# Performance work log

Hardware: AMD Instinct MI355X
Metric: run time of the kernel (lower is better)

## Reference

```python
import jax, jax.numpy as jnp
import numpy as np

B, V, L, D, H, W = 4, 2, 8192, 768, 12, 512  # batch, views, seq, d_model, heads, window


def _layernorm(x, g, b, eps=1e-5):
    # matches torch LayerNorm computed in fp32 then cast back
    x32 = x.astype(jnp.float32)
    m = x32.mean(-1, keepdims=True)
    v = ((x32 - m) ** 2).mean(-1, keepdims=True)
    return ((x32 - m) * jax.lax.rsqrt(v + eps) * g + b).astype(x.dtype)


def _mha(q_in, k_in, v_in, wqkv, bqkv, wo, bo, h):
    # torch nn.MultiheadAttention (eval mode, no mask). inputs [..., S, d]
    d = q_in.shape[-1]
    hd = d // h
    scale = 1.0 / np.sqrt(hd)
    q = (q_in @ wqkv[:d].T + bqkv[:d]).reshape(*q_in.shape[:-1], h, hd)
    k = (k_in @ wqkv[d:2 * d].T + bqkv[d:2 * d]).reshape(*k_in.shape[:-1], h, hd)
    v = (v_in @ wqkv[2 * d:].T + bqkv[2 * d:]).reshape(*v_in.shape[:-1], h, hd)
    scores = jnp.einsum('...qhd,...khd->...hqk', q, k) * scale
    a = jax.nn.softmax(scores, axis=-1)
    o = jnp.einsum('...hqk,...khd->...qhd', a, v).reshape(q_in.shape)
    return o @ wo.T + bo


def reference(x, ln1_g, ln1_b, ln2_g, ln2_b,
              a1_wqkv, a1_bqkv, a1_wo, a1_bo,
              a2_wqkv, a2_bqkv, a2_wo, a2_bo,
              fc_w, fc_b, proj_w, proj_b, index):
    b, v, l, c = x.shape
    y = _layernorm(x, ln1_g, ln1_b)
    shifted = (index % 2 == 1)  # index is a static Python int
    xs = jnp.roll(x, W // 2, axis=2) if shifted else x
    p = l // W
    xw = xs.reshape(b, v, p, W, c)  # window partition (only x is rolled, as in source)
    yw = y.reshape(b, v, p, W, c)
    # cross-view windowed attention: Q=norm view i, K=norm view j, V=raw view i
    v1 = _mha(yw[:, 0], yw[:, 1], xw[:, 0], a1_wqkv, a1_bqkv, a1_wo, a1_bo, H)
    v2 = _mha(yw[:, 1], yw[:, 0], xw[:, 1], a2_wqkv, a2_bqkv, a2_wo, a2_bo, H)
    att = jnp.stack([v1, v2], axis=1).reshape(b, v, l, c)
    if shifted:
        att = jnp.roll(att, -(W // 2), axis=2)
    x = x + att
    y2 = _layernorm(x, ln2_g, ln2_b)
    h = y2 @ fc_w.T + fc_b
    h = h * jax.nn.sigmoid(1.702 * h)  # fast GELU
    return x + (h @ proj_w.T + proj_b)


def setup_inputs() -> dict:
    key = jax.random.key(0)
    ks = jax.random.split(key, 10)
    s = 0.02
    return {
        'x': jax.random.normal(ks[0], (B, V, L, D), jnp.float32),
        'ln1_g': jnp.ones((D,), jnp.float32),
        'ln1_b': jnp.zeros((D,), jnp.float32),
        'ln2_g': jnp.ones((D,), jnp.float32),
        'ln2_b': jnp.zeros((D,), jnp.float32),
        'a1_wqkv': jax.random.normal(ks[1], (3 * D, D), jnp.float32) * s,
        'a1_bqkv': jnp.zeros((3 * D,), jnp.float32),
        'a1_wo': jax.random.normal(ks[2], (D, D), jnp.float32) * s,
        'a1_bo': jnp.zeros((D,), jnp.float32),
        'a2_wqkv': jax.random.normal(ks[3], (3 * D, D), jnp.float32) * s,
        'a2_bqkv': jnp.zeros((3 * D,), jnp.float32),
        'a2_wo': jax.random.normal(ks[4], (D, D), jnp.float32) * s,
        'a2_bo': jnp.zeros((D,), jnp.float32),
        'fc_w': jax.random.normal(ks[5], (4 * D, D), jnp.float32) * s,
        'fc_b': jnp.zeros((4 * D,), jnp.float32),
        'proj_w': jax.random.normal(ks[6], (D, 4 * D), jnp.float32) * s,
        'proj_b': jnp.zeros((D,), jnp.float32),
        'index': 0,
    }
```

## Files before the change

### kernel.cpp

```cpp
#include <hip/hip_runtime.h>
#include <hip/hip_bf16.h>

typedef __bf16 bf16x8 __attribute__((ext_vector_type(8)));
typedef float  f32x4  __attribute__((ext_vector_type(4)));
typedef short  s16x4  __attribute__((ext_vector_type(4)));
typedef unsigned short u16;

#define L2E 1.44269504088896f

static __device__ __forceinline__ u16 f2bf(float f) {
  unsigned u = __builtin_bit_cast(unsigned, f);
  u += 0x7fffu + ((u >> 16) & 1u);
  return (u16)(u >> 16);
}

static __device__ __forceinline__ void gld_lds16(const void* g, void* l) {
  __builtin_amdgcn_global_load_lds((const __attribute__((address_space(1))) unsigned*)g,
                                   (__attribute__((address_space(3))) unsigned*)l, 16, 0, 0);
}

__global__ __launch_bounds__(256)
void cvtk(const float* __restrict__ s, u16* __restrict__ d, int n) {
  const int i = (blockIdx.x * 256 + threadIdx.x) * 4;
  if (i >= n) return;
  const float4 f = *(const float4*)(s + i);
  s16x4 p;
  p[0] = (short)f2bf(f.x); p[1] = (short)f2bf(f.y);
  p[2] = (short)f2bf(f.z); p[3] = (short)f2bf(f.w);
  *(s16x4*)(d + i) = p;
}

__global__ __launch_bounds__(256)
void lnk(const float* __restrict__ x, const float* __restrict__ gw,
         const float* __restrict__ bw, u16* __restrict__ y,
         u16* __restrict__ xv, int viewmajor) {
  const int lane = threadIdx.x & 63;
  const int tok = blockIdx.x * 4 + (threadIdx.x >> 6);
  const float* xr = x + (size_t)tok * 768;
  float4 v[3];
  float s = 0.f, sq = 0.f;
#pragma unroll
  for (int j = 0; j < 3; ++j) {
    v[j] = *(const float4*)(xr + j * 256 + lane * 4);
    s  += v[j].x + v[j].y + v[j].z + v[j].w;
    sq += v[j].x * v[j].x + v[j].y * v[j].y + v[j].z * v[j].z + v[j].w * v[j].w;
  }
#pragma unroll
  for (int o = 1; o < 64; o <<= 1) { s += __shfl_xor(s, o); sq += __shfl_xor(sq, o); }
  const float mean = s * (1.f / 768.f);
  const float var  = sq * (1.f / 768.f) - mean * mean;
  const float rstd = rsqrtf(var + 1e-5f);
  size_t yrow = (size_t)tok;
  if (viewmajor) {
    const int b_ = tok >> 14, vv = (tok >> 13) & 1, l_ = tok & 8191;
    yrow = ((size_t)((vv << 2) + b_) << 13) + l_;
  }
#pragma unroll
  for (int j = 0; j < 3; ++j) {
    const float4 g4 = *(const float4*)(gw + j * 256 + lane * 4);
    const float4 b4 = *(const float4*)(bw + j * 256 + lane * 4);
    s16x4 py;
    py[0] = (short)f2bf((v[j].x - mean) * rstd * g4.x + b4.x);
    py[1] = (short)f2bf((v[j].y - mean) * rstd * g4.y + b4.y);
    py[2] = (short)f2bf((v[j].z - mean) * rstd * g4.z + b4.z);
    py[3] = (short)f2bf((v[j].w - mean) * rstd * g4.w + b4.w);
    *(s16x4*)(y + yrow * 768 + j * 256 + lane * 4) = py;
    if (xv) {
      s16x4 px;
      px[0] = (short)f2bf(v[j].x); px[1] = (short)f2bf(v[j].y);
      px[2] = (short)f2bf(v[j].z); px[3] = (short)f2bf(v[j].w);
      *(s16x4*)(xv + yrow * 768 + j * 256 + lane * 4) = px;
    }
  }
}

template<int MODE>
__global__ __launch_bounds__(512, 2)
void gemm_bt(const u16* __restrict__ A, const u16* __restrict__ B,
             const float* __restrict__ bias, void* __restrict__ Cp,
             int N, int K,
             const float* __restrict__ xres, const int* __restrict__ idxp,
             int vview) {
  __shared__ char lds[131072];
  const int t = threadIdx.x;
  const int lane = t & 63;
  const int wid = t >> 6;
  const int wm = wid >> 2, wn = wid & 3;

  const int cpx = gridDim.x >> 3;
  const int bid = (blockIdx.x & 7) * cpx + (blockIdx.x >> 3);

  const int Ntiles = N >> 8;
  const int PPB = Ntiles << 3;
  const int panel = bid / PPB;
  const int rem = bid - panel * PPB;
  const int nt = rem >> 3;
  const int mt = (panel << 3) + (rem & 7);

  const int ra = t >> 3;
  const int sc = ((t & 7) ^ (ra & 7)) << 3;
  const u16* Asrc = A + (size_t)(mt * 256 + ra) * K + sc;
  const u16* Bsrc = B + (size_t)(nt * 256 + ra) * K + sc;
  char* LA = (char*)lds;
  char* LB = (char*)lds + 65536;
  const int wdst = wid << 10;

  auto stageA = [&](int d, int kt) {
#pragma unroll
    for (int h = 0; h < 2; ++h) {
      const u16* s = Asrc + (size_t)kt * 64 + (size_t)(h * 128) * K;
      char* dst = LA + (d * 2 + h) * 16384 + wdst;
      gld_lds16(s, dst);
      gld_lds16(s + (size_t)64 * K, dst + 8192);
    }
  };
  auto stageB = [&](int d, int kt) {
#pragma unroll
    for (int h = 0; h < 2; ++h) {
      const u16* s = Bsrc + (size_t)kt * 64 + (size_t)(h * 128) * K;
      char* dst = LB + (d * 2 + h) * 16384 + wdst;
      gld_lds16(s, dst);
      gld_lds16(s + (size_t)64 * K, dst + 8192);
    }
  };

  const int c15 = lane & 15;
  const int swz = (lane & 7) << 4;
  const int cb0 = (((lane >> 4) << 4)) ^ swz;
  const int cb1 = (64 | ((lane >> 4) << 4)) ^ swz;
  const int bofs = (wn & 1) * 64;

  f32x4 acc[8][4] = {};
  const int nk = K >> 6;

  stageA(0, 0); stageB(0, 0);
  asm volatile("s_waitcnt vmcnt(0)" ::: "memory");
  __builtin_amdgcn_s_barrier();
  __builtin_amdgcn_sched_barrier(0);

  for (int kt = 0; kt < nk; ++kt) {
    const int d = kt & 1;
    if (kt + 1 < nk) { stageA(d ^ 1, kt + 1); stageB(d ^ 1, kt + 1); }
    __builtin_amdgcn_sched_barrier(0);

    const char* lA = LA + (d * 2 + wm) * 16384;
    const char* lB = LB + (d * 2 + (wn >> 1)) * 16384;

    auto rdA = [&](bf16x8 (&av)[4][2], int mh) {
#pragma unroll
      for (int m = 0; m < 4; ++m) {
        const char* r = lA + (mh * 64 + m * 16 + c15) * 128;
        av[m][0] = *(const bf16x8*)(r + cb0);
        av[m][1] = *(const bf16x8*)(r + cb1);
      }
    };
    auto rdB = [&](bf16x8 (&bv)[2][2], int nh) {
#pragma unroll
      for (int n = 0; n < 2; ++n) {
        const char* r = lB + (bofs + nh * 32 + n * 16 + c15) * 128;
        bv[n][0] = *(const bf16x8*)(r + cb0);
        bv[n][1] = *(const bf16x8*)(r + cb1);
      }
    };
    auto mm = [&](bf16x8 (&av)[4][2], bf16x8 (&bv)[2][2], int mq, int nq) {
      __builtin_amdgcn_s_setprio(1);
#pragma unroll
      for (int ks = 0; ks < 2; ++ks)
#pragma unroll
        for (int m = 0; m < 4; ++m)
#pragma unroll
          for (int n = 0; n < 2; ++n)
            acc[mq * 4 + m][nq * 2 + n] = __builtin_amdgcn_mfma_f32_16x16x32_bf16(
                av[m][ks], bv[n][ks], acc[mq * 4 + m][nq * 2 + n], 0, 0, 0);
      __builtin_amdgcn_s_setprio(0);
    };

    bf16x8 av[4][2], bv[2][2];
    rdA(av, 0); rdB(bv, 0); mm(av, bv, 0, 0);
    rdB(bv, 1);             mm(av, bv, 0, 1);
    rdA(av, 1);             mm(av, bv, 1, 1);
    rdB(bv, 0);             mm(av, bv, 1, 0);

    asm volatile("s_waitcnt vmcnt(0)" ::: "memory");
    __builtin_amdgcn_s_barrier();
    __builtin_amdgcn_sched_barrier(0);
  }

  int shift = 0;
  if constexpr (MODE == 2) shift = (idxp[0] & 1) ? 256 : 0;

  const int rb0 = mt * 256 + wm * 128 + ((lane >> 4) << 2);
  const int cbase = nt * 256 + wn * 64 + c15;
#pragma unroll
  for (int mi = 0; mi < 8; ++mi) {
    const int row = rb0 + mi * 16;
#pragma unroll
    for (int nj = 0; nj < 4; ++nj) {
      const int col = cbase + nj * 16;
      const float bv = bias[col];
      if constexpr (MODE == 0) {
        u16* C = (u16*)Cp;
#pragma unroll
        for (int r = 0; r < 4; ++r)
          C[(size_t)(row + r) * N + col] = f2bf(acc[mi][nj][r] + bv);
      } else if constexpr (MODE == 1) {
        u16* C = (u16*)Cp;
        const int hh = col >> 6, dd = col & 63;
        const int b_ = row >> 13, l_ = row & 8191;
        s16x4 pk;
#pragma unroll
        for (int r = 0; r < 4; ++r) pk[r] = (short)f2bf(acc[mi][nj][r] + bv);
        *(s16x4*)(C + (((size_t)((b_ * 12 + hh) << 6) + dd) << 13) + l_) = pk;
      } else if constexpr (MODE == 2) {
        float* C = (float*)Cp;
        const int b_ = row >> 13, p_ = row & 8191;
        const int l0 = (p_ - shift) & 8191;
        const size_t rbase = ((size_t)((b_ << 1) + vview) << 13) + l0;
#pragma unroll
        for (int r = 0; r < 4; ++r) {
          const size_t idx = (rbase + r) * 768 + col;
          C[idx] = xres[idx] + acc[mi][nj][r] + bv;
        }
      } else if constexpr (MODE == 3) {
        u16* C = (u16*)Cp;
#pragma unroll
        for (int r = 0; r < 4; ++r) {
          const float u = acc[mi][nj][r] + bv;
          const float e = __builtin_amdgcn_exp2f(-2.45546693f * u);
          C[(size_t)(row + r) * N + col] = f2bf(u / (1.f + e));
        }
      } else {
        float* C = (float*)Cp;
#pragma unroll
        for (int r = 0; r < 4; ++r) {
          const size_t idx = (size_t)(row + r) * 768 + col;
          C[idx] = C[idx] + acc[mi][nj][r] + bv;
        }
      }
    }
  }
}

__global__ __launch_bounds__(256)
void attnk(const u16* __restrict__ Q1, const u16* __restrict__ K1, const u16* __restrict__ V1,
           const u16* __restrict__ Q2, const u16* __restrict__ K2, const u16* __restrict__ V2,
           u16* __restrict__ O, const int* __restrict__ idxp) {
  const int lane = threadIdx.x & 63;
  const int c = lane & 15, g = lane >> 4;
  const int unit = blockIdx.x * 4 + (threadIdx.x >> 6);
  const int qc = unit & 7;
  int u2 = unit >> 3;
  const int h = u2 % 12; u2 /= 12;
  const int w = u2 & 15; u2 >>= 4;
  const int b = u2 & 3;
  const int a = u2 >> 2;
  const int shift = (idxp[0] & 1) ? 256 : 0;

  const u16* Q  = a ? Q2 : Q1;
  const u16* Kb = a ? K2 : K1;
  const u16* Vt = a ? V2 : V1;

  const int qrow0 = b * 8192 + w * 512 + qc * 64;
  bf16x8 qf[4][2];
#pragma unroll
  for (int q = 0; q < 4; ++q)
#pragma unroll
    for (int hf = 0; hf < 2; ++hf)
      qf[q][hf] = *(const bf16x8*)(Q + (size_t)(qrow0 + q * 16 + c) * 768 + h * 64 + hf * 32 + g * 8);

  f32x4 oacc[4][4] = {};
  f32x4 psum[4] = {};
  const short* Vts = (const short*)Vt + (((size_t)((b * 12 + h) << 6)) << 13);
  const int kbase = b * 8192 + w * 512;
  const float CEXP = 0.125f * L2E;

  for (int kt = 0; kt < 32; ++kt) {
    const size_t krow = (size_t)(kbase + kt * 16 + c) * 768 + h * 64 + g * 8;
    const bf16x8 kf0 = *(const bf16x8*)(Kb + krow);
    const bf16x8 kf1 = *(const bf16x8*)(Kb + krow + 32);
    const int lv = (w * 512 + kt * 16 + g * 4 - shift) & 8191;
    s16x4 vf[4];
#pragma unroll
    for (int df = 0; df < 4; ++df)
      vf[df] = *(const s16x4*)(Vts + ((size_t)(df * 16 + c) << 13) + lv);

    const f32x4 z = {0.f, 0.f, 0.f, 0.f};
    s16x4 pk[4];
#pragma unroll
    for (int q = 0; q < 4; ++q) {
      f32x4 sc2 = __builtin_amdgcn_mfma_f32_16x16x32_bf16(kf0, qf[q][0], z, 0, 0, 0);
      sc2 = __builtin_amdgcn_mfma_f32_16x16x32_bf16(kf1, qf[q][1], sc2, 0, 0, 0);
      f32x4 pv;
      pv[0] = __builtin_amdgcn_exp2f(sc2[0] * CEXP);
      pv[1] = __builtin_amdgcn_exp2f(sc2[1] * CEXP);
      pv[2] = __builtin_amdgcn_exp2f(sc2[2] * CEXP);
      pv[3] = __builtin_amdgcn_exp2f(sc2[3] * CEXP);
      psum[q] += pv;
      pk[q][0] = (short)f2bf(pv[0]);
      pk[q][1] = (short)f2bf(pv[1]);
      pk[q][2] = (short)f2bf(pv[2]);
      pk[q][3] = (short)f2bf(pv[3]);
    }
#pragma unroll
    for (int df = 0; df < 4; ++df)
#pragma unroll
      for (int q = 0; q < 4; ++q)
        oacc[df][q] = __builtin_amdgcn_mfma_f32_16x16x16bf16_1k(vf[df], pk[q], oacc[df][q], 0, 0, 0);
  }

  const size_t orow0 = (size_t)(a * 32768 + qrow0);
#pragma unroll
  for (int q = 0; q < 4; ++q) {
    float ss = psum[q][0] + psum[q][1] + psum[q][2] + psum[q][3];
    ss += __shfl_xor(ss, 16);
    ss += __shfl_xor(ss, 32);
    const float inv = 1.f / ss;
#pragma unroll
    for (int df = 0; df < 4; ++df) {
      s16x4 po;
#pragma unroll
      for (int r = 0; r < 4; ++r) po[r] = (short)f2bf(oacc[df][q][r] * inv);
      *(s16x4*)(O + (orow0 + q * 16 + c) * 768 + h * 64 + df * 16 + g * 4) = po;
    }
  }
}

extern "C" void kernel_launch(void* const* d_in, const int* in_sizes, int n_in,
                              void* d_out, int out_size, void* d_ws, size_t ws_size,
                              hipStream_t stream) {
  const float* x       = (const float*)d_in[0];
  const float* ln1_g   = (const float*)d_in[1];
  const float* ln1_b   = (const float*)d_in[2];
  const float* ln2_g   = (const float*)d_in[3];
  const float* ln2_b   = (const float*)d_in[4];
  const float* a1_wqkv = (const float*)d_in[5];
  const float* a1_bqkv = (const float*)d_in[6];
  const float* a1_wo   = (const float*)d_in[7];
  const float* a1_bo   = (const float*)d_in[8];
  const float* a2_wqkv = (const float*)d_in[9];
  const float* a2_bqkv = (const float*)d_in[10];
  const float* a2_wo   = (const float*)d_in[11];
  const float* a2_bo   = (const float*)d_in[12];
  const float* fc_w    = (const float*)d_in[13];
  const float* fc_b    = (const float*)d_in[14];
  const float* proj_w  = (const float*)d_in[15];
  const float* proj_b  = (const float*)d_in[16];
  const int*   idxp    = (const int*)d_in[17];
  float* out = (float*)d_out;

  u16* p = (u16*)d_ws;
  u16* w1  = p; p += (size_t)2304 * 768;
  u16* w2  = p; p += (size_t)2304 * 768;
  u16* wo1 = p; p += (size_t)768 * 768;
  u16* wo2 = p; p += (size_t)768 * 768;
  u16* fcw = p; p += (size_t)3072 * 768;
  u16* pjw = p; p += (size_t)768 * 3072;
  u16* y   = p; p += (size_t)65536 * 768;
  u16* xv  = p; p += (size_t)65536 * 768;
  u16* Q1  = p; p += (size_t)32768 * 768;
  u16* K1  = p; p += (size_t)32768 * 768;
  u16* V1  = p; p += (size_t)32768 * 768;
  u16* Q2  = p; p += (size_t)32768 * 768;
  u16* K2  = p; p += (size_t)32768 * 768;
  u16* V2  = p; p += (size_t)32768 * 768;
  u16* Ob  = p; p += (size_t)65536 * 768;
  u16* hb  = Q1;

  cvtk<<<1728, 256, 0, stream>>>(a1_wqkv, w1, 2304 * 768);
  cvtk<<<1728, 256, 0, stream>>>(a2_wqkv, w2, 2304 * 768);
  cvtk<<<576,  256, 0, stream>>>(a1_wo, wo1, 768 * 768);
  cvtk<<<576,  256, 0, stream>>>(a2_wo, wo2, 768 * 768);
  cvtk<<<2304, 256, 0, stream>>>(fc_w, fcw, 3072 * 768);
  cvtk<<<2304, 256, 0, stream>>>(proj_w, pjw, 768 * 3072);

  lnk<<<16384, 256, 0, stream>>>(x, ln1_g, ln1_b, y, xv, 1);

  const size_t VS = (size_t)32768 * 768;
  gemm_bt<0><<<384, 512, 0, stream>>>(y,        w1,                  a1_bqkv,        Q1, 768, 768, nullptr, nullptr, 0);
  gemm_bt<0><<<384, 512, 0, stream>>>(y + VS,   w1 + 768 * 768,      a1_bqkv + 768,  K1, 768, 768, nullptr, nullptr, 0);
  gemm_bt<1><<<384, 512, 0, stream>>>(xv,       w1 + 2 * 768 * 768,  a1_bqkv + 1536, V1, 768, 768, nullptr, nullptr, 0);
  gemm_bt<0><<<384, 512, 0, stream>>>(y + VS,   w2,                  a2_bqkv,        Q2, 768, 768, nullptr, nullptr, 0);
  gemm_bt<0><<<384, 512, 0, stream>>>(y,        w2 + 768 * 768,      a2_bqkv + 768,  K2, 768, 768, nullptr, nullptr, 0);
  gemm_bt<1><<<384, 512, 0, stream>>>(xv + VS,  w2 + 2 * 768 * 768,  a2_bqkv + 1536, V2, 768, 768, nullptr, nullptr, 0);

  attnk<<<3072, 256, 0, stream>>>(Q1, K1, V1, Q2, K2, V2, Ob, idxp);

  gemm_bt<2><<<384, 512, 0, stream>>>(Ob,      wo1, a1_bo, out, 768, 768, x, idxp, 0);
  gemm_bt<2><<<384, 512, 0, stream>>>(Ob + VS, wo2, a2_bo, out, 768, 768, x, idxp, 1);

  lnk<<<16384, 256, 0, stream>>>(out, ln2_g, ln2_b, y, nullptr, 0);

  gemm_bt<3><<<3072, 512, 0, stream>>>(y, fcw, fc_b, hb, 3072, 768, nullptr, nullptr, 0);

  gemm_bt<4><<<768, 512, 0, stream>>>(hb, pjw, proj_b, out, 768, 3072, nullptr, nullptr, 0);
}
```

Baseline: 1.666 ms.

## Restructure GEMM main loop into 4-slot ring buffer with K=32 steps

The bf16 MFMA GEMM main loop moves from a double-buffered K=64 tile to a four-slot LDS ring of K=32 tiles with a prefetch distance of two. Partial vmcnt waits leave later prefetches in flight, and there is a single barrier per iteration. The LDS layout changes to column-chunk-major 16-byte rows without XOR swizzle, so each wave loads all eight A and four B fragments at once before issuing 32 MFMAs. The aim is to hide global-to-LDS latency better and remove the interleaved read/compute staging, at the cost of twice as many barriers and loop iterations.

```diff
diff --git a/kernel.cpp b/kernel.cpp
--- a/kernel.cpp
+++ b/kernel.cpp
@@ -97,93 +97,58 @@
   const int nt = rem >> 3;
   const int mt = (panel << 3) + (rem & 7);
 
-  const int ra = t >> 3;
-  const int sc = ((t & 7) ^ (ra & 7)) << 3;
-  const u16* Asrc = A + (size_t)(mt * 256 + ra) * K + sc;
-  const u16* Bsrc = B + (size_t)(nt * 256 + ra) * K + sc;
-  char* LA = (char*)lds;
-  char* LB = (char*)lds + 65536;
-  const int wdst = wid << 10;
-
-  auto stageA = [&](int d, int kt) {
-#pragma unroll
-    for (int h = 0; h < 2; ++h) {
-      const u16* s = Asrc + (size_t)kt * 64 + (size_t)(h * 128) * K;
-      char* dst = LA + (d * 2 + h) * 16384 + wdst;
-      gld_lds16(s, dst);
-      gld_lds16(s + (size_t)64 * K, dst + 8192);
-    }
+  const int sch = wid >> 2;
+  const int srow = (wid & 3) * 64 + lane;
+  const u16* Asrc = A + (size_t)(mt * 256 + srow) * K;
+  const u16* Bsrc = B + (size_t)(nt * 256 + srow) * K;
+  const int wdst = (wid << 10);
+
+  auto stage = [&](int slot, int kt) {
+    char* base = (char*)lds + slot * 32768;
+#pragma unroll
+    for (int i = 0; i < 2; ++i)
+      gld_lds16(Asrc + kt * 32 + (i * 2 + sch) * 8, base + i * 8192 + wdst);
+#pragma unroll
+    for (int i = 0; i < 2; ++i)
+      gld_lds16(Bsrc + kt * 32 + (i * 2 + sch) * 8, base + 16384 + i * 8192 + wdst);
   };
-  auto stageB = [&](int d, int kt) {
-#pragma unroll
-    for (int h = 0; h < 2; ++h) {
-      const u16* s = Bsrc + (size_t)kt * 64 + (size_t)(h * 128) * K;
-      char* dst = LB + (d * 2 + h) * 16384 + wdst;
-      gld_lds16(s, dst);
-      gld_lds16(s + (size_t)64 * K, dst + 8192);
-    }
-  };
 
   const int c15 = lane & 15;
-  const int swz = (lane & 7) << 4;
-  const int cb0 = (((lane >> 4) << 4)) ^ swz;
-  const int cb1 = (64 | ((lane >> 4) << 4)) ^ swz;
-  const int bofs = (wn & 1) * 64;
+  const int g16 = (lane >> 4) << 12;
 
   f32x4 acc[8][4] = {};
-  const int nk = K >> 6;
-
-  stageA(0, 0); stageB(0, 0);
-  asm volatile("s_waitcnt vmcnt(0)" ::: "memory");
-  __builtin_amdgcn_s_barrier();
-  __builtin_amdgcn_sched_barrier(0);
+  const int nk = K >> 5;
+
+  stage(0, 0);
+  stage(1, 1);
 
   for (int kt = 0; kt < nk; ++kt) {
-    const int d = kt & 1;
-    if (kt + 1 < nk) { stageA(d ^ 1, kt + 1); stageB(d ^ 1, kt + 1); }
+    const int slot = kt & 3;
+    if (kt + 2 < nk) stage((kt + 2) & 3, kt + 2);
     __builtin_amdgcn_sched_barrier(0);
-
-    const char* lA = LA + (d * 2 + wm) * 16384;
-    const char* lB = LB + (d * 2 + (wn >> 1)) * 16384;
-
-    auto rdA = [&](bf16x8 (&av)[4][2], int mh) {
-#pragma unroll
-      for (int m = 0; m < 4; ++m) {
-        const char* r = lA + (mh * 64 + m * 16 + c15) * 128;
-        av[m][0] = *(const bf16x8*)(r + cb0);
-        av[m][1] = *(const bf16x8*)(r + cb1);
-      }
-    };
-    auto rdB = [&](bf16x8 (&bv)[2][2], int nh) {
-#pragma unroll
-      for (int n = 0; n < 2; ++n) {
-        const char* r = lB + (bofs + nh * 32 + n * 16 + c15) * 128;
-        bv[n][0] = *(const bf16x8*)(r + cb0);
-        bv[n][1] = *(const bf16x8*)(r + cb1);
-      }
-    };
-    auto mm = [&](bf16x8 (&av)[4][2], bf16x8 (&bv)[2][2], int mq, int nq) {
-      __builtin_amdgcn_s_setprio(1);
-#pragma unroll
-      for (int ks = 0; ks < 2; ++ks)
-#pragma unroll
-        for (int m = 0; m < 4; ++m)
-#pragma unroll
-          for (int n = 0; n < 2; ++n)
-            acc[mq * 4 + m][nq * 2 + n] = __builtin_amdgcn_mfma_f32_16x16x32_bf16(
-                av[m][ks], bv[n][ks], acc[mq * 4 + m][nq * 2 + n], 0, 0, 0);
-      __builtin_amdgcn_s_setprio(0);
-    };
-
-    bf16x8 av[4][2], bv[2][2];
-    rdA(av, 0); rdB(bv, 0); mm(av, bv, 0, 0);
-    rdB(bv, 1);             mm(av, bv, 0, 1);
-    rdA(av, 1);             mm(av, bv, 1, 1);
-    rdB(bv, 0);             mm(av, bv, 1, 0);
-
-    asm volatile("s_waitcnt vmcnt(0)" ::: "memory");
+    if (kt + 2 < nk)      asm volatile("s_waitcnt vmcnt(8)" ::: "memory");
+    else if (kt + 1 < nk) asm volatile("s_waitcnt vmcnt(4)" ::: "memory");
+    else                  asm volatile("s_waitcnt vmcnt(0)" ::: "memory");
     __builtin_amdgcn_s_barrier();
     __builtin_amdgcn_sched_barrier(0);
+
+    const char* LA = (char*)lds + slot * 32768 + g16;
+    const char* LB = LA + 16384;
+    bf16x8 av[8], bv[4];
+#pragma unroll
+    for (int m = 0; m < 8; ++m)
+      av[m] = *(const bf16x8*)(LA + (wm * 128 + m * 16 + c15) * 16);
+#pragma unroll
+    for (int n = 0; n < 4; ++n)
+      bv[n] = *(const bf16x8*)(LB + (wn * 64 + n * 16 + c15) * 16);
+
+    __builtin_amdgcn_s_setprio(1);
+#pragma unroll
+    for (int m = 0; m < 8; ++m)
+#pragma unroll
+      for (int n = 0; n < 4; ++n)
+        acc[m][n] = __builtin_amdgcn_mfma_f32_16x16x32_bf16(av[m], bv[n], acc[m][n], 0, 0, 0);
+    __builtin_amdgcn_s_setprio(0);
   }
 
   int shift = 0;
```

New measurement: 2.323 ms. +39.5%, slower.
